# Kernel optimization log

Measured on AMD Instinct MI355X. Metric: run time of the kernel, lower is better.

The kernel has to match this reference:

```python
import jax, jax.numpy as jnp
import numpy as np

MASK_VALUE = -1e30


def setup_inputs() -> dict:
    key = jax.random.key(0)
    ks = jax.random.split(key, 8)
    B, N, M, D = 64, 1024, 128, 256
    c = jax.random.normal(ks[0], (B, N, D), dtype=jnp.float32)
    q = jax.random.normal(ks[1], (B, M, D), dtype=jnp.float32)
    c_mask = jax.random.randint(ks[2], (B, N), 0, 2, dtype=jnp.int32)
    q_mask = jax.random.randint(ks[3], (B, M), 0, 2, dtype=jnp.int32)
    w0 = jax.random.normal(ks[4], (D, 1), dtype=jnp.float32) * 0.06  # glorot-ish scale
    w1 = jax.random.normal(ks[5], (D, 1), dtype=jnp.float32) * 0.06
    wm = jax.random.normal(ks[6], (D,), dtype=jnp.float32) * 0.06
    bias = jnp.zeros((M,), dtype=jnp.float32)
    return {"c": c, "q": q, "c_mask": c_mask, "q_mask": q_mask,
            "w0": w0, "w1": w1, "wm": wm, "bias": bias}


def reference(c, q, c_mask, q_mask, w0, w1, wm, bias):
    # Trilinear similarity S[b,i,j] = c.w0 + q.w1 + sum_d c*wm*q + bias[j]
    sub0 = jnp.einsum('bnd,do->bno', c, w0)              # (B,N,1)
    sub1 = jnp.einsum('bmd,do->bom', q, w1)              # (B,1,M)
    sub2 = jnp.einsum('bnd,d,bmd->bnm', c, wm, q)        # (B,N,M)
    S = sub0 + sub1 + sub2 + bias                        # bias broadcast over last axis
    qm = q_mask.astype(jnp.float32)[:, None, :]          # (B,1,M)
    cm = c_mask.astype(jnp.float32)[:, :, None]          # (B,N,1)
    S_ = jax.nn.softmax(S + MASK_VALUE * (1.0 - qm), axis=-1)   # row softmax over query
    S_T = jnp.swapaxes(jax.nn.softmax(S + MASK_VALUE * (1.0 - cm), axis=1), 1, 2)  # (B,M,N)
    c2q = jnp.matmul(S_, q)                              # (B,N,D)
    q2c = jnp.matmul(jnp.matmul(S_, S_T), c)             # (B,N,D)
    return jnp.concatenate([c, c2q, c * c2q, c * q2c], axis=-1)  # (B,N,4D)
```

## Files before the change

kernel.cpp:

```cpp
#include <hip/hip_runtime.h>
#include <cfloat>

#define BB 64
#define NN 1024
#define MM 128
#define DD 256
#define MASKV (-1e30f)

typedef __attribute__((ext_vector_type(8))) short bf16x8;
typedef __attribute__((ext_vector_type(16))) float f32x16;

__device__ __forceinline__ unsigned short f2bf(float x) {
  union { float f; unsigned int u; } v; v.f = x;
  unsigned int r = v.u + 0x7fffu + ((v.u >> 16) & 1u);
  return (unsigned short)(r >> 16);
}
__device__ __forceinline__ float bf2f(unsigned short h) {
  union { float f; unsigned int u; } v; v.u = ((unsigned int)h) << 16;
  return v.f;
}
__device__ __forceinline__ void split8(const float* xs, uint4* hv, uint4* lv) {
  unsigned hp[4], lp[4];
  #pragma unroll
  for (int p = 0; p < 4; p++) {
    unsigned short h0 = f2bf(xs[2 * p]), h1 = f2bf(xs[2 * p + 1]);
    unsigned short g0 = f2bf(xs[2 * p] - bf2f(h0));
    unsigned short g1 = f2bf(xs[2 * p + 1] - bf2f(h1));
    hp[p] = (unsigned)h0 | ((unsigned)h1 << 16);
    lp[p] = (unsigned)g0 | ((unsigned)g1 << 16);
  }
  *hv = make_uint4(hp[0], hp[1], hp[2], hp[3]);
  *lv = make_uint4(lp[0], lp[1], lp[2], lp[3]);
}
__device__ __forceinline__ bf16x8 u2b(uint4 u) {
  union { uint4 a; bf16x8 b; } x; x.a = u; return x.b;
}

__global__ __launch_bounds__(256) void k_dots(
    const float* __restrict__ c, const float* __restrict__ q,
    const int* __restrict__ qmask,
    const float* __restrict__ w0, const float* __restrict__ w1,
    const float* __restrict__ bias,
    float* __restrict__ sub0, float* __restrict__ qtermM) {
  int wave = (blockIdx.x * blockDim.x + threadIdx.x) >> 6;
  int lane = threadIdx.x & 63;
  const int total = BB * NN + BB * MM;
  if (wave >= total) return;
  const float* row;
  const float* w;
  if (wave < BB * NN) { row = c + (size_t)wave * DD; w = w0; }
  else                { row = q + (size_t)(wave - BB * NN) * DD; w = w1; }
  float4 v  = *(const float4*)(row + lane * 4);
  float4 wv = *(const float4*)(w   + lane * 4);
  float s = v.x * wv.x + v.y * wv.y + v.z * wv.z + v.w * wv.w;
  #pragma unroll
  for (int off = 32; off > 0; off >>= 1) s += __shfl_xor(s, off, 64);
  if (lane == 0) {
    if (wave < BB * NN) {
      sub0[wave] = s;
    } else {
      int r = wave - BB * NN;
      int m = r & (MM - 1);
      qtermM[r] = s + bias[m] + (qmask[r] ? 0.0f : MASKV);
    }
  }
}

__global__ __launch_bounds__(256) void k_zero(float* __restrict__ p) {
  p[blockIdx.x * 256 + threadIdx.x] = 0.0f;
}

__global__ __launch_bounds__(256) void k_score(
    const float* __restrict__ c, const float* __restrict__ q,
    const int* __restrict__ cmask, const float* __restrict__ wm,
    const float* __restrict__ sub0, const float* __restrict__ qtermM,
    float* __restrict__ S_, float* __restrict__ E,
    float* __restrict__ colsum) {
  __shared__ unsigned short cwh[128 * 64];
  __shared__ unsigned short cwl[128 * 64];
  __shared__ unsigned short qhi[128 * 64];
  __shared__ unsigned short qlo[128 * 64];
  const int b = blockIdx.y;
  const int n0 = blockIdx.x * 128;
  const int t = threadIdx.x;
  const int w = t >> 6;
  const int l = t & 63;
  const int l31 = l & 31;
  const int lh = l >> 5;

  f32x16 acc[4];
  #pragma unroll
  for (int mb = 0; mb < 4; mb++)
    #pragma unroll
    for (int i = 0; i < 16; i++) acc[mb][i] = 0.0f;

  for (int k0 = 0; k0 < DD; k0 += 64) {
    __syncthreads();
    #pragma unroll
    for (int g = 0; g < 4; g++) {
      int lin = t + g * 256;
      int row = lin >> 3;
      int kg  = (lin & 7) * 8;
      unsigned boff = (unsigned)(row * 128 + ((kg * 2) ^ ((row & 7) << 4)));
      float4 w0v = *(const float4*)(wm + k0 + kg);
      float4 w1v = *(const float4*)(wm + k0 + kg + 4);
      const float* cp = c + (size_t)(b * NN + n0 + row) * DD + k0 + kg;
      float4 a0 = *(const float4*)cp;
      float4 a1 = *(const float4*)(cp + 4);
      float xs[8] = {a0.x * w0v.x, a0.y * w0v.y, a0.z * w0v.z, a0.w * w0v.w,
                     a1.x * w1v.x, a1.y * w1v.y, a1.z * w1v.z, a1.w * w1v.w};
      uint4 hv, lv;
      split8(xs, &hv, &lv);
      *(uint4*)((char*)cwh + boff) = hv;
      *(uint4*)((char*)cwl + boff) = lv;
      const float* qp = q + (size_t)(b * MM + row) * DD + k0 + kg;
      float4 b0 = *(const float4*)qp;
      float4 b1 = *(const float4*)(qp + 4);
      float ys[8] = {b0.x, b0.y, b0.z, b0.w, b1.x, b1.y, b1.z, b1.w};
      split8(ys, &hv, &lv);
      *(uint4*)((char*)qhi + boff) = hv;
      *(uint4*)((char*)qlo + boff) = lv;
    }
    __syncthreads();
    #pragma unroll
    for (int ks = 0; ks < 64; ks += 16) {
      int ak = ks + lh * 8;
      unsigned arow = (unsigned)(w * 32 + l31);
      unsigned aoff = arow * 128 + (((unsigned)(ak * 2)) ^ ((arow & 7) << 4));
      bf16x8 ah = *(const bf16x8*)((const char*)cwh + aoff);
      bf16x8 al = *(const bf16x8*)((const char*)cwl + aoff);
      #pragma unroll
      for (int mb = 0; mb < 4; mb++) {
        unsigned brow = (unsigned)(mb * 32 + l31);
        unsigned boff2 = brow * 128 + (((unsigned)(ak * 2)) ^ ((brow & 7) << 4));
        bf16x8 bh = *(const bf16x8*)((const char*)qhi + boff2);
        bf16x8 bl = *(const bf16x8*)((const char*)qlo + boff2);
        acc[mb] = __builtin_amdgcn_mfma_f32_32x32x16_bf16(ah, bh, acc[mb], 0, 0, 0);
        acc[mb] = __builtin_amdgcn_mfma_f32_32x32x16_bf16(ah, bl, acc[mb], 0, 0, 0);
        acc[mb] = __builtin_amdgcn_mfma_f32_32x32x16_bf16(al, bh, acc[mb], 0, 0, 0);
      }
    }
  }

  float qt[4];
  #pragma unroll
  for (int mb = 0; mb < 4; mb++) qt[mb] = qtermM[b * MM + mb * 32 + l31];

  float ps[4] = {0.f, 0.f, 0.f, 0.f};
  #pragma unroll
  for (int r = 0; r < 16; r++) {
    int row = (r & 3) + 8 * (r >> 2) + 4 * lh;
    int gn = n0 + w * 32 + row;
    float s0m = sub0[b * NN + gn] + (cmask[b * NN + gn] ? 0.0f : MASKV);
    float x[4];
    float vmax = -FLT_MAX;
    #pragma unroll
    for (int mb = 0; mb < 4; mb++) { x[mb] = acc[mb][r] + qt[mb]; vmax = fmaxf(vmax, x[mb]); }
    #pragma unroll
    for (int off = 16; off > 0; off >>= 1) vmax = fmaxf(vmax, __shfl_xor(vmax, off, 64));
    float e[4];
    float vsum = 0.0f;
    #pragma unroll
    for (int mb = 0; mb < 4; mb++) { e[mb] = __expf(x[mb] - vmax); vsum += e[mb]; }
    #pragma unroll
    for (int off = 16; off > 0; off >>= 1) vsum += __shfl_xor(vsum, off, 64);
    float inv = 1.0f / vsum;
    size_t base = (size_t)(b * NN + gn) * MM + l31;
    #pragma unroll
    for (int mb = 0; mb < 4; mb++) {
      S_[base + mb * 32] = e[mb] * inv;
      float Ev = __expf(acc[mb][r] + s0m);
      E[base + mb * 32] = Ev;
      ps[mb] += Ev;
    }
  }
  #pragma unroll
  for (int mb = 0; mb < 4; mb++) {
    ps[mb] += __shfl_xor(ps[mb], 32, 64);
    if (lh == 0) atomicAdd(&colsum[b * MM + mb * 32 + l31], ps[mb]);
  }
}

__global__ __launch_bounds__(256) void k_colA(
    const float* __restrict__ E, const float* __restrict__ c,
    const float* __restrict__ colsum, float* __restrict__ A) {
  __shared__ float se[32 * 64];
  __shared__ float sc[32 * 64];
  const int b = blockIdx.z;
  const int m0 = blockIdx.x * 64;
  const int d0 = blockIdx.y * 64;
  const int t = threadIdx.x;
  const int tx = t & 15;
  const int ty = t >> 4;
  const int lr = t >> 4;
  const int lc = (t & 15) * 4;

  const float* Eb = E + (size_t)b * NN * MM + m0 + lc;
  const float* cb = c + (size_t)b * NN * DD + d0 + lc;

  float4 ev0 = *(const float4*)(Eb + (size_t)lr * MM);
  float4 ev1 = *(const float4*)(Eb + (size_t)(16 + lr) * MM);
  float4 cv0 = *(const float4*)(cb + (size_t)lr * DD);
  float4 cv1 = *(const float4*)(cb + (size_t)(16 + lr) * DD);

  float acc[4][4];
  #pragma unroll
  for (int mi = 0; mi < 4; mi++)
    #pragma unroll
    for (int di = 0; di < 4; di++) acc[mi][di] = 0.0f;

  for (int n0 = 0; n0 < NN; n0 += 32) {
    *(float4*)(&se[lr * 64 + lc])        = ev0;
    *(float4*)(&se[(16 + lr) * 64 + lc]) = ev1;
    *(float4*)(&sc[lr * 64 + lc])        = cv0;
    *(float4*)(&sc[(16 + lr) * 64 + lc]) = cv1;
    __syncthreads();
    if (n0 + 32 < NN) {
      int nn = n0 + 32;
      ev0 = *(const float4*)(Eb + (size_t)(nn + lr) * MM);
      ev1 = *(const float4*)(Eb + (size_t)(nn + 16 + lr) * MM);
      cv0 = *(const float4*)(cb + (size_t)(nn + lr) * DD);
      cv1 = *(const float4*)(cb + (size_t)(nn + 16 + lr) * DD);
    }
    #pragma unroll
    for (int kk = 0; kk < 32; kk++) {
      float4 e4 = *(const float4*)(&se[kk * 64 + ty * 4]);
      float4 c4 = *(const float4*)(&sc[kk * 64 + tx * 4]);
      float em[4] = {e4.x, e4.y, e4.z, e4.w};
      float cd[4] = {c4.x, c4.y, c4.z, c4.w};
      #pragma unroll
      for (int mi = 0; mi < 4; mi++)
        #pragma unroll
        for (int di = 0; di < 4; di++) acc[mi][di] += em[mi] * cd[di];
    }
    __syncthreads();
  }

  #pragma unroll
  for (int mi = 0; mi < 4; mi++) {
    int m = m0 + ty * 4 + mi;
    float inv = 1.0f / colsum[b * MM + m];
    float4 o = make_float4(acc[mi][0] * inv, acc[mi][1] * inv,
                           acc[mi][2] * inv, acc[mi][3] * inv);
    *(float4*)(A + (size_t)(b * MM + m) * DD + d0 + tx * 4) = o;
  }
}

__global__ __launch_bounds__(512) void k_out(
    const float* __restrict__ c, const float* __restrict__ q,
    const float* __restrict__ S_, const float* __restrict__ A,
    float* __restrict__ out) {
  const int b = blockIdx.y;
  const int n0 = blockIdx.x * 64;
  const int t = threadIdx.x;
  const int w = t >> 6;
  const int l = t & 63;
  const int l31 = l & 31;
  const int lh = l >> 5;
  const int grp = w >> 2;
  const int wi = w & 3;
  const int nf = wi & 1;
  const int fd0 = (wi >> 1) * 4;

  const float* Bsrc = grp ? A : q;

  f32x16 acc[4];
  #pragma unroll
  for (int df = 0; df < 4; df++)
    #pragma unroll
    for (int i = 0; i < 16; i++) acc[df][i] = 0.0f;

  const float* srow = S_ + (size_t)(b * NN + n0 + nf * 32 + l31) * MM + lh * 8;
  const float* bbase = Bsrc + (size_t)(b * MM + lh * 8) * DD + l31;

  #pragma unroll 2
  for (int ks = 0; ks < 8; ks++) {
    float4 s0 = *(const float4*)(srow + ks * 16);
    float4 s1 = *(const float4*)(srow + ks * 16 + 4);
    float xs[8] = {s0.x, s0.y, s0.z, s0.w, s1.x, s1.y, s1.z, s1.w};
    uint4 hv, lv;
    split8(xs, &hv, &lv);
    bf16x8 ah = u2b(hv), al = u2b(lv);
    #pragma unroll
    for (int df = 0; df < 4; df++) {
      const float* bp = bbase + (size_t)(ks * 16) * DD + (fd0 + df) * 32;
      float ys[8];
      #pragma unroll
      for (int j = 0; j < 8; j++) ys[j] = bp[j * DD];
      split8(ys, &hv, &lv);
      bf16x8 bh = u2b(hv), bl = u2b(lv);
      acc[df] = __builtin_amdgcn_mfma_f32_32x32x16_bf16(ah, bh, acc[df], 0, 0, 0);
      acc[df] = __builtin_amdgcn_mfma_f32_32x32x16_bf16(ah, bl, acc[df], 0, 0, 0);
      acc[df] = __builtin_amdgcn_mfma_f32_32x32x16_bf16(al, bh, acc[df], 0, 0, 0);
    }
  }

  #pragma unroll
  for (int df = 0; df < 4; df++) {
    int d = (fd0 + df) * 32 + l31;
    #pragma unroll
    for (int r = 0; r < 16; r++) {
      int row = (r & 3) + 8 * (r >> 2) + 4 * lh;
      int gn = n0 + nf * 32 + row;
      float v = acc[df][r];
      float cv = c[(size_t)(b * NN + gn) * DD + d];
      size_t ob = (size_t)(b * NN + gn) * (4 * DD) + d;
      if (grp == 0) {
        out[ob]            = cv;
        out[ob + DD]       = v;
        out[ob + 2 * DD]   = cv * v;
      } else {
        out[ob + 3 * DD]   = cv * v;
      }
    }
  }
}

extern "C" void kernel_launch(void* const* d_in, const int* in_sizes, int n_in,
                              void* d_out, int out_size, void* d_ws, size_t ws_size,
                              hipStream_t stream) {
  const float* c     = (const float*)d_in[0];
  const float* q     = (const float*)d_in[1];
  const int*   cmask = (const int*)d_in[2];
  const int*   qmask = (const int*)d_in[3];
  const float* w0    = (const float*)d_in[4];
  const float* w1    = (const float*)d_in[5];
  const float* wm    = (const float*)d_in[6];
  const float* bias  = (const float*)d_in[7];
  float* out = (float*)d_out;
  float* ws  = (float*)d_ws;

  float* S_     = ws;
  float* E      = ws + 8388608;
  float* A      = ws + 16777216;
  float* sub0   = ws + 18874368;
  float* qtermM = ws + 18939904;
  float* colsum = ws + 18948096;

  k_dots<<<18432, 256, 0, stream>>>(c, q, qmask, w0, w1, bias, sub0, qtermM);
  k_zero<<<32, 256, 0, stream>>>(colsum);
  k_score<<<dim3(8, BB), 256, 0, stream>>>(c, q, cmask, wm, sub0, qtermM, S_, E, colsum);
  k_colA<<<dim3(2, 4, BB), 256, 0, stream>>>(E, c, colsum, A);
  k_out<<<dim3(16, BB), 512, 0, stream>>>(c, q, S_, A, out);
}
```

Before: 509.1 us.

## Move column-softmax weighted sum to split-bf16 MFMA with transposed E and split-K

```diff
diff --git a/kernel.cpp b/kernel.cpp
--- a/kernel.cpp
+++ b/kernel.cpp
@@ -74,7 +74,8 @@
     const float* __restrict__ c, const float* __restrict__ q,
     const int* __restrict__ cmask, const float* __restrict__ wm,
     const float* __restrict__ sub0, const float* __restrict__ qtermM,
-    float* __restrict__ S_, float* __restrict__ E,
+    float* __restrict__ S_,
+    unsigned short* __restrict__ EThi, unsigned short* __restrict__ ETlo,
     float* __restrict__ colsum) {
   __shared__ unsigned short cwh[128 * 64];
   __shared__ unsigned short cwl[128 * 64];
@@ -148,30 +149,49 @@
 
   float ps[4] = {0.f, 0.f, 0.f, 0.f};
   #pragma unroll
-  for (int r = 0; r < 16; r++) {
-    int row = (r & 3) + 8 * (r >> 2) + 4 * lh;
-    int gn = n0 + w * 32 + row;
-    float s0m = sub0[b * NN + gn] + (cmask[b * NN + gn] ? 0.0f : MASKV);
-    float x[4];
-    float vmax = -FLT_MAX;
-    #pragma unroll
-    for (int mb = 0; mb < 4; mb++) { x[mb] = acc[mb][r] + qt[mb]; vmax = fmaxf(vmax, x[mb]); }
-    #pragma unroll
-    for (int off = 16; off > 0; off >>= 1) vmax = fmaxf(vmax, __shfl_xor(vmax, off, 64));
-    float e[4];
-    float vsum = 0.0f;
-    #pragma unroll
-    for (int mb = 0; mb < 4; mb++) { e[mb] = __expf(x[mb] - vmax); vsum += e[mb]; }
-    #pragma unroll
-    for (int off = 16; off > 0; off >>= 1) vsum += __shfl_xor(vsum, off, 64);
-    float inv = 1.0f / vsum;
-    size_t base = (size_t)(b * NN + gn) * MM + l31;
+  for (int g = 0; g < 4; g++) {
+    float evg[4][4];
+    #pragma unroll
+    for (int j = 0; j < 4; j++) {
+      int r = 4 * g + j;
+      int row = j + 8 * g + 4 * lh;
+      int gn = n0 + w * 32 + row;
+      float s0m = sub0[b * NN + gn] + (cmask[b * NN + gn] ? 0.0f : MASKV);
+      float x[4];
+      float vmax = -FLT_MAX;
+      #pragma unroll
+      for (int mb = 0; mb < 4; mb++) { x[mb] = acc[mb][r] + qt[mb]; vmax = fmaxf(vmax, x[mb]); }
+      #pragma unroll
+      for (int off = 16; off > 0; off >>= 1) vmax = fmaxf(vmax, __shfl_xor(vmax, off, 64));
+      float e[4];
+      float vsum = 0.0f;
+      #pragma unroll
+      for (int mb = 0; mb < 4; mb++) { e[mb] = __expf(x[mb] - vmax); vsum += e[mb]; }
+      #pragma unroll
+      for (int off = 16; off > 0; off >>= 1) vsum += __shfl_xor(vsum, off, 64);
+      float inv = 1.0f / vsum;
+      size_t base = (size_t)(b * NN + gn) * MM + l31;
+      #pragma unroll
+      for (int mb = 0; mb < 4; mb++) {
+        S_[base + mb * 32] = e[mb] * inv;
+        float Ev = __expf(acc[mb][r] + s0m);
+        evg[mb][j] = Ev;
+        ps[mb] += Ev;
+      }
+    }
     #pragma unroll
     for (int mb = 0; mb < 4; mb++) {
-      S_[base + mb * 32] = e[mb] * inv;
-      float Ev = __expf(acc[mb][r] + s0m);
-      E[base + mb * 32] = Ev;
-      ps[mb] += Ev;
+      unsigned short h[4], lo[4];
+      #pragma unroll
+      for (int j = 0; j < 4; j++) {
+        h[j] = f2bf(evg[mb][j]);
+        lo[j] = f2bf(evg[mb][j] - bf2f(h[j]));
+      }
+      size_t off = (size_t)(b * MM + mb * 32 + l31) * NN + n0 + w * 32 + 8 * g + 4 * lh;
+      *(uint2*)(EThi + off) = make_uint2((unsigned)h[0] | ((unsigned)h[1] << 16),
+                                         (unsigned)h[2] | ((unsigned)h[3] << 16));
+      *(uint2*)(ETlo + off) = make_uint2((unsigned)lo[0] | ((unsigned)lo[1] << 16),
+                                         (unsigned)lo[2] | ((unsigned)lo[3] << 16));
     }
   }
   #pragma unroll
@@ -181,69 +201,73 @@
   }
 }
 
-__global__ __launch_bounds__(256) void k_colA(
-    const float* __restrict__ E, const float* __restrict__ c,
-    const float* __restrict__ colsum, float* __restrict__ A) {
-  __shared__ float se[32 * 64];
-  __shared__ float sc[32 * 64];
-  const int b = blockIdx.z;
-  const int m0 = blockIdx.x * 64;
-  const int d0 = blockIdx.y * 64;
+__global__ __launch_bounds__(512) void k_colA(
+    const unsigned short* __restrict__ EThi, const unsigned short* __restrict__ ETlo,
+    const float* __restrict__ c, float* __restrict__ Apart) {
+  const int p = blockIdx.x;
+  const int b = blockIdx.y;
   const int t = threadIdx.x;
-  const int tx = t & 15;
-  const int ty = t >> 4;
-  const int lr = t >> 4;
-  const int lc = (t & 15) * 4;
-
-  const float* Eb = E + (size_t)b * NN * MM + m0 + lc;
-  const float* cb = c + (size_t)b * NN * DD + d0 + lc;
-
-  float4 ev0 = *(const float4*)(Eb + (size_t)lr * MM);
-  float4 ev1 = *(const float4*)(Eb + (size_t)(16 + lr) * MM);
-  float4 cv0 = *(const float4*)(cb + (size_t)lr * DD);
-  float4 cv1 = *(const float4*)(cb + (size_t)(16 + lr) * DD);
-
-  float acc[4][4];
-  #pragma unroll
-  for (int mi = 0; mi < 4; mi++)
-    #pragma unroll
-    for (int di = 0; di < 4; di++) acc[mi][di] = 0.0f;
-
-  for (int n0 = 0; n0 < NN; n0 += 32) {
-    *(float4*)(&se[lr * 64 + lc])        = ev0;
-    *(float4*)(&se[(16 + lr) * 64 + lc]) = ev1;
-    *(float4*)(&sc[lr * 64 + lc])        = cv0;
-    *(float4*)(&sc[(16 + lr) * 64 + lc]) = cv1;
-    __syncthreads();
-    if (n0 + 32 < NN) {
-      int nn = n0 + 32;
-      ev0 = *(const float4*)(Eb + (size_t)(nn + lr) * MM);
-      ev1 = *(const float4*)(Eb + (size_t)(nn + 16 + lr) * MM);
-      cv0 = *(const float4*)(cb + (size_t)(nn + lr) * DD);
-      cv1 = *(const float4*)(cb + (size_t)(nn + 16 + lr) * DD);
-    }
-    #pragma unroll
-    for (int kk = 0; kk < 32; kk++) {
-      float4 e4 = *(const float4*)(&se[kk * 64 + ty * 4]);
-      float4 c4 = *(const float4*)(&sc[kk * 64 + tx * 4]);
-      float em[4] = {e4.x, e4.y, e4.z, e4.w};
-      float cd[4] = {c4.x, c4.y, c4.z, c4.w};
-      #pragma unroll
-      for (int mi = 0; mi < 4; mi++)
-        #pragma unroll
-        for (int di = 0; di < 4; di++) acc[mi][di] += em[mi] * cd[di];
-    }
-    __syncthreads();
-  }
-
-  #pragma unroll
-  for (int mi = 0; mi < 4; mi++) {
-    int m = m0 + ty * 4 + mi;
-    float inv = 1.0f / colsum[b * MM + m];
-    float4 o = make_float4(acc[mi][0] * inv, acc[mi][1] * inv,
-                           acc[mi][2] * inv, acc[mi][3] * inv);
-    *(float4*)(A + (size_t)(b * MM + m) * DD + d0 + tx * 4) = o;
-  }
+  const int w = t >> 6;
+  const int l = t & 63;
+  const int l31 = l & 31, lh = l >> 5;
+  const int d = w * 32 + l31;
+
+  f32x16 acc[4];
+  #pragma unroll
+  for (int mf = 0; mf < 4; mf++)
+    #pragma unroll
+    for (int i = 0; i < 16; i++) acc[mf][i] = 0.0f;
+
+  const float* cb = c + (size_t)b * NN * DD + d;
+  const size_t etb = (size_t)b * MM * NN + (size_t)p * 256 + lh * 8;
+
+  for (int ks = 0; ks < 16; ks++) {
+    int nb = p * 256 + ks * 16 + lh * 8;
+    float ys[8];
+    #pragma unroll
+    for (int j = 0; j < 8; j++) ys[j] = cb[(size_t)(nb + j) * DD];
+    uint4 hv, lv;
+    split8(ys, &hv, &lv);
+    bf16x8 ah = u2b(hv), al = u2b(lv);
+    #pragma unroll
+    for (int mf = 0; mf < 4; mf++) {
+      size_t eoff = etb + (size_t)(mf * 32 + l31) * NN + ks * 16;
+      bf16x8 bh = *(const bf16x8*)(EThi + eoff);
+      bf16x8 bl = *(const bf16x8*)(ETlo + eoff);
+      acc[mf] = __builtin_amdgcn_mfma_f32_32x32x16_bf16(ah, bh, acc[mf], 0, 0, 0);
+      acc[mf] = __builtin_amdgcn_mfma_f32_32x32x16_bf16(ah, bl, acc[mf], 0, 0, 0);
+      acc[mf] = __builtin_amdgcn_mfma_f32_32x32x16_bf16(al, bh, acc[mf], 0, 0, 0);
+    }
+  }
+
+  float* ap = Apart + (size_t)p * (BB * MM * DD);
+  #pragma unroll
+  for (int mf = 0; mf < 4; mf++) {
+    size_t rowb = (size_t)(b * MM + mf * 32 + l31) * DD + w * 32 + 4 * lh;
+    #pragma unroll
+    for (int g = 0; g < 4; g++) {
+      float4 o = make_float4(acc[mf][4 * g + 0], acc[mf][4 * g + 1],
+                             acc[mf][4 * g + 2], acc[mf][4 * g + 3]);
+      *(float4*)(ap + rowb + 8 * g) = o;
+    }
+  }
+}
+
+__global__ __launch_bounds__(256) void k_reduceA(
+    const float* __restrict__ Apart, const float* __restrict__ colsum,
+    float* __restrict__ A) {
+  int f = blockIdx.x * 256 + threadIdx.x;
+  const float4* p0 = (const float4*)Apart + f;
+  float4 a0 = p0[0];
+  float4 a1 = p0[524288];
+  float4 a2 = p0[1048576];
+  float4 a3 = p0[1572864];
+  float inv = 1.0f / colsum[f >> 6];
+  float4 o = make_float4((a0.x + a1.x + a2.x + a3.x) * inv,
+                         (a0.y + a1.y + a2.y + a3.y) * inv,
+                         (a0.z + a1.z + a2.z + a3.z) * inv,
+                         (a0.w + a1.w + a2.w + a3.w) * inv);
+  ((float4*)A)[f] = o;
 }
 
 __global__ __launch_bounds__(512) void k_out(
@@ -331,15 +355,18 @@
   float* ws  = (float*)d_ws;
 
   float* S_     = ws;
-  float* E      = ws + 8388608;
-  float* A      = ws + 16777216;
-  float* sub0   = ws + 18874368;
-  float* qtermM = ws + 18939904;
-  float* colsum = ws + 18948096;
+  unsigned short* EThi = (unsigned short*)(ws + 8388608);
+  unsigned short* ETlo = (unsigned short*)(ws + 12582912);
+  float* Apart  = ws + 16777216;
+  float* A      = ws + 25165824;
+  float* sub0   = ws + 27262976;
+  float* qtermM = ws + 27328512;
+  float* colsum = ws + 27336704;
 
   k_dots<<<18432, 256, 0, stream>>>(c, q, qmask, w0, w1, bias, sub0, qtermM);
   k_zero<<<32, 256, 0, stream>>>(colsum);
-  k_score<<<dim3(8, BB), 256, 0, stream>>>(c, q, cmask, wm, sub0, qtermM, S_, E, colsum);
-  k_colA<<<dim3(2, 4, BB), 256, 0, stream>>>(E, c, colsum, A);
+  k_score<<<dim3(8, BB), 256, 0, stream>>>(c, q, cmask, wm, sub0, qtermM, S_, EThi, ETlo, colsum);
+  k_colA<<<dim3(4, BB), 512, 0, stream>>>(EThi, ETlo, c, Apart);
+  k_reduceA<<<2048, 256, 0, stream>>>(Apart, colsum, A);
   k_out<<<dim3(16, BB), 512, 0, stream>>>(c, q, S_, A, out);
 }
```

Measured after the change: 543.2 us. 1.07x slower.
